# Performance work log

Measured on AMD Instinct MI355X. Metric: run time of the kernel, lower is better.

Reference implementation:

```python
import jax, jax.numpy as jnp
import numpy as np

V, E, H, B, S = 50257, 1024, 1024, 32, 1024

def setup_inputs() -> dict:
    key = jax.random.key(0)
    ks = jax.random.split(key, 16)
    s = 0.02
    return {
        "word_inputs": jax.random.randint(ks[0], (B, 1), 0, V),
        "hidden": jax.random.normal(ks[1], (1, B, H), jnp.float32),
        "output_encoder": jax.random.normal(ks[2], (B, S, H), jnp.float32),
        "emb": jax.random.normal(ks[3], (V, E), jnp.float32) * 0.2,
        "W_a1": jax.random.normal(ks[4], (H, 2 * H), jnp.float32) * s,
        "b_a1": jnp.zeros((H,), jnp.float32),
        "W_a2": jax.random.normal(ks[5], (1, H), jnp.float32) * s,
        "b_a2": jnp.zeros((1,), jnp.float32),
        "W_c": jax.random.normal(ks[6], (H, 2 * H), jnp.float32) * s,
        "b_c": jnp.zeros((H,), jnp.float32),
        "W_ih": jax.random.normal(ks[7], (3 * H, E), jnp.float32) * s,
        "W_hh": jax.random.normal(ks[8], (3 * H, H), jnp.float32) * s,
        "b_ih": jnp.zeros((3 * H,), jnp.float32),
        "b_hh": jnp.zeros((3 * H,), jnp.float32),
        "W_fc": jax.random.normal(ks[9], (V, H), jnp.float32) * 0.2,
        "b_fc": jnp.zeros((V,), jnp.float32),
    }

def reference(word_inputs, hidden, output_encoder, emb, W_a1, b_a1, W_a2, b_a2,
              W_c, b_c, W_ih, W_hh, b_ih, b_hh, W_fc, b_fc):
    b, s, h = output_encoder.shape
    h_prev = hidden[0]                                      # [B,H]
    # Bahdanau additive attention, vectorized over all S timesteps
    eh = jnp.concatenate(
        [output_encoder, jnp.broadcast_to(h_prev[:, None, :], (b, s, h))],
        axis=-1)                                            # [B,S,2H]
    scores = jnp.tanh(jnp.einsum('bsk,hk->bsh', eh, W_a1) + b_a1)
    scores = (jnp.einsum('bsh,oh->bso', scores, W_a2) + b_a2)[..., 0]  # [B,S]
    attn = jax.nn.softmax(scores, axis=1)                   # [B,S]
    context = jnp.einsum('bs,bsh->bh', attn, output_encoder)  # [B,H]
    embedded = emb[word_inputs.reshape(-1)]                 # [B,E]
    ec = jnp.concatenate([embedded, context], axis=-1)      # [B,E+H]
    x = jax.nn.relu(ec @ W_c.T + b_c)                       # [B,H]
    # single-step GRU (PyTorch gate order: r, z, n)
    gi = x @ W_ih.T + b_ih                                  # [B,3H]
    gh = h_prev @ W_hh.T + b_hh                             # [B,3H]
    i_r, i_z, i_n = jnp.split(gi, 3, axis=-1)
    h_r, h_z, h_n = jnp.split(gh, 3, axis=-1)
    r = jax.nn.sigmoid(i_r + h_r)
    z = jax.nn.sigmoid(i_z + h_z)
    n = jnp.tanh(i_n + r * h_n)
    h_new = (1.0 - z) * n + z * h_prev                      # [B,H]
    out = jax.nn.relu(h_new) @ W_fc.T + b_fc                # [B,V]
    return out, h_new[None, :, :]
```

## Files before the change

kernel.cpp:

```cpp
#include <hip/hip_runtime.h>

#define B_  32
#define S_  1024
#define H_  1024
#define V_  50257

typedef __attribute__((ext_vector_type(8))) short bf16x8;
typedef __attribute__((ext_vector_type(4))) float f32x4;
typedef __attribute__((ext_vector_type(8))) unsigned short u16x8;

__device__ __forceinline__ unsigned short f2b(float f) {
  union { float f; unsigned u; } v; v.f = f;
  unsigned r = 0x7FFFu + ((v.u >> 16) & 1u);
  return (unsigned short)((v.u + r) >> 16);
}
__device__ __forceinline__ float b2f(unsigned short h) {
  union { unsigned u; float f; } v; v.u = ((unsigned)h) << 16;
  return v.f;
}

__device__ __forceinline__ void async16(void* lds, const void* g) {
  typedef __attribute__((address_space(3))) void as3_void;
  typedef __attribute__((address_space(1))) void as1_void;
  as3_void* l = (as3_void*)(unsigned)(unsigned long long)lds;
  const as1_void* s = (const as1_void*)(unsigned long long)g;
  __builtin_amdgcn_global_load_lds(s, l, 16, 0, 0);
}

__global__ void prologue_kernel(const float* __restrict__ enc, unsigned short* __restrict__ enc_bf,
                                const float* __restrict__ wa1, const float* __restrict__ hidden,
                                const float* __restrict__ b_a1,
                                unsigned short* __restrict__ wa1_bf, float* __restrict__ part2) {
  __shared__ float wrow[H_];
  int tid = threadIdx.x;
  if (blockIdx.x < 16384) {
    size_t i = ((size_t)blockIdx.x * 256 + tid) * 8;
    float4 v0 = *(const float4*)(enc + i);
    float4 v1 = *(const float4*)(enc + i + 4);
    u16x8 o;
    o[0]=f2b(v0.x); o[1]=f2b(v0.y); o[2]=f2b(v0.z); o[3]=f2b(v0.w);
    o[4]=f2b(v1.x); o[5]=f2b(v1.y); o[6]=f2b(v1.z); o[7]=f2b(v1.w);
    *(u16x8*)(enc_bf + i) = o;
    return;
  }
  int h = blockIdx.x - 16384;
  {
    int c = tid * 4;
    float4 v = *(const float4*)(wa1 + (size_t)h * 2048 + c);
    ushort4 o;
    o.x = f2b(v.x); o.y = f2b(v.y); o.z = f2b(v.z); o.w = f2b(v.w);
    *(ushort4*)(wa1_bf + (size_t)h * 1024 + c) = o;
  }
  {
    int c = tid * 4;
    float4 v = *(const float4*)(wa1 + (size_t)h * 2048 + 1024 + c);
    wrow[c] = v.x; wrow[c+1] = v.y; wrow[c+2] = v.z; wrow[c+3] = v.w;
  }
  __syncthreads();
  int wave = tid >> 6, lane = tid & 63;
  float bias = b_a1[h];
  for (int bb = 0; bb < 8; ++bb) {
    int b = wave * 8 + bb;
    float acc = 0.f;
    for (int k = lane; k < H_; k += 64) acc += wrow[k] * hidden[b * H_ + k];
    #pragma unroll
    for (int off = 32; off; off >>= 1) acc += __shfl_xor(acc, off);
    if (lane == 0) part2[b * H_ + h] = acc + bias;
  }
}

__global__ __launch_bounds__(256) void scores_m97(
    const unsigned short* __restrict__ A,
    const unsigned short* __restrict__ Bm,
    const float* __restrict__ part2,
    const float* __restrict__ wa2,
    float* __restrict__ partials)
{
  __shared__ __align__(16) unsigned short As[2048];
  __shared__ __align__(16) unsigned short Bs[4096];
  const int tid = threadIdx.x;
  const int wave = tid >> 6, lane = tid & 63;
  const int wr = wave >> 1, wc = wave & 1;
  const int l15 = lane & 15, l16 = lane >> 4;

  const int id = blockIdx.x;
  const int xcd = id & 7;
  const int s = id >> 3;
  const int bm = (s >> 3) * 8 + xcd;
  const int bn = s & 7;

  const unsigned short* Abase = A  + (size_t)(bm * 64) * 1024;
  const unsigned short* Bbase = Bm + (size_t)(bn * 128) * 1024;

  const int Lc = tid * 16;
  const int r0 = Lc >> 6;
  const int ce0 = ((Lc & 63) ^ (((r0 >> 1) & 3) << 4)) >> 1;

  f32x4 acc[2][4];
  #pragma unroll
  for (int mi = 0; mi < 2; ++mi)
    #pragma unroll
    for (int ni = 0; ni < 4; ++ni) acc[mi][ni] = (f32x4){0.f, 0.f, 0.f, 0.f};
  bf16x8 af[2], bfr[4];

  for (int kt = 0; kt < 1024; kt += 32) {
    async16((char*)As + Lc,        Abase + (size_t)r0 * 1024 + kt + ce0);
    async16((char*)Bs + Lc,        Bbase + (size_t)r0 * 1024 + kt + ce0);
    async16((char*)Bs + Lc + 4096, Bbase + (size_t)(r0 + 64) * 1024 + kt + ce0);
    asm volatile("s_waitcnt vmcnt(0)" ::: "memory");
    __syncthreads();
    #pragma unroll
    for (int mi = 0; mi < 2; ++mi) {
      int ar = wr * 32 + mi * 16 + l15;
      int L = ar * 64 + l16 * 16;
      af[mi] = *(const bf16x8*)((const char*)As + (L ^ (((ar >> 1) & 3) << 4)));
    }
    #pragma unroll
    for (int ni = 0; ni < 4; ++ni) {
      int br = wc * 64 + ni * 16 + l15;
      int L = br * 64 + l16 * 16;
      bfr[ni] = *(const bf16x8*)((const char*)Bs + (L ^ (((br >> 1) & 3) << 4)));
    }
    #pragma unroll
    for (int mi = 0; mi < 2; ++mi)
      #pragma unroll
      for (int ni = 0; ni < 4; ++ni)
        acc[mi][ni] = __builtin_amdgcn_mfma_f32_16x16x32_bf16(af[mi], bfr[ni], acc[mi][ni], 0, 0, 0);
    __syncthreads();
  }

  const int b = bm >> 4;
  float w2[4], p2[4];
  #pragma unroll
  for (int ni = 0; ni < 4; ++ni) {
    int col = bn * 128 + wc * 64 + ni * 16 + l15;
    w2[ni] = wa2[col];
    p2[ni] = part2[b * H_ + col];
  }
  #pragma unroll
  for (int mi = 0; mi < 2; ++mi) {
    #pragma unroll
    for (int r = 0; r < 4; ++r) {
      float s2 = 0.f;
      #pragma unroll
      for (int ni = 0; ni < 4; ++ni)
        s2 += w2[ni] * tanhf(acc[mi][ni][r] + p2[ni]);
      s2 += __shfl_xor(s2, 1); s2 += __shfl_xor(s2, 2);
      s2 += __shfl_xor(s2, 4); s2 += __shfl_xor(s2, 8);
      if (l15 == 0) {
        int row = bm * 64 + wr * 32 + mi * 16 + l16 * 4 + r;
        partials[(size_t)row * 16 + bn * 2 + wc] = s2;
      }
    }
  }
}

__global__ __launch_bounds__(256) void smctx_kernel(
    const float* __restrict__ partials, const unsigned short* __restrict__ encbf,
    float* __restrict__ ctxp) {
  int sc = blockIdx.x, b = blockIdx.y, tid = threadIdx.x;
  int lane = tid & 63, wid = tid >> 6;
  __shared__ float att[1024];
  __shared__ float red[4];
  float scv[4];
  float mx = -1e30f;
  #pragma unroll
  for (int j = 0; j < 4; ++j) {
    int r = tid * 4 + j;
    const float4* p = (const float4*)(partials + ((size_t)b * 1024 + r) * 16);
    float s = 0.f;
    #pragma unroll
    for (int i = 0; i < 4; ++i) { float4 v = p[i]; s += v.x + v.y + v.z + v.w; }
    scv[j] = s; mx = fmaxf(mx, s);
  }
  #pragma unroll
  for (int off = 32; off; off >>= 1) mx = fmaxf(mx, __shfl_xor(mx, off));
  if (lane == 0) red[wid] = mx;
  __syncthreads();
  float M = fmaxf(fmaxf(red[0], red[1]), fmaxf(red[2], red[3]));
  float ssum = 0.f;
  #pragma unroll
  for (int j = 0; j < 4; ++j) { float e = expf(scv[j] - M); att[tid*4+j] = e; ssum += e; }
  #pragma unroll
  for (int off = 32; off; off >>= 1) ssum += __shfl_xor(ssum, off);
  __syncthreads();
  if (lane == 0) red[wid] = ssum;
  __syncthreads();
  float inv = 1.f / (red[0] + red[1] + red[2] + red[3]);
  int h4 = tid * 4;
  float a0 = 0, a1 = 0, a2 = 0, a3 = 0;
  const unsigned short* base = encbf + (size_t)b * S_ * H_ + h4;
  #pragma unroll 4
  for (int i = 0; i < 64; ++i) {
    float w = att[sc * 64 + i] * inv;
    ushort4 ev = *(const ushort4*)(base + (size_t)(sc * 64 + i) * H_);
    a0 += w * b2f(ev.x); a1 += w * b2f(ev.y); a2 += w * b2f(ev.z); a3 += w * b2f(ev.w);
  }
  float4 o = {a0, a1, a2, a3};
  *(float4*)(ctxp + (size_t)(sc * B_ + b) * H_ + h4) = o;
}

__global__ __launch_bounds__(256) void wc_gemm(
    const int* __restrict__ word, const float* __restrict__ emb,
    const float* __restrict__ ctxp, const float* __restrict__ Wc,
    float* __restrict__ xp) {
  int nb = blockIdx.x, kc = blockIdx.y, tid = threadIdx.x;
  __shared__ unsigned short A_lds[32][136];
  {
    int b = tid >> 3, cg = tid & 7;
    int c0 = cg * 16;
    if (kc < 8) {
      int w = word[b];
      const float* er = emb + (size_t)w * H_ + kc * 128 + c0;
      #pragma unroll
      for (int c = 0; c < 16; c += 4) {
        float4 v = *(const float4*)(er + c);
        ushort4 o; o.x = f2b(v.x); o.y = f2b(v.y); o.z = f2b(v.z); o.w = f2b(v.w);
        *(ushort4*)&A_lds[b][c0 + c] = o;
      }
    } else {
      int h0 = (kc - 8) * 128 + c0;
      #pragma unroll
      for (int c = 0; c < 16; c += 4) {
        float s0 = 0, s1 = 0, s2 = 0, s3 = 0;
        #pragma unroll
        for (int sc = 0; sc < 16; ++sc) {
          float4 v = *(const float4*)(ctxp + ((size_t)(sc * B_ + b)) * H_ + h0 + c);
          s0 += v.x; s1 += v.y; s2 += v.z; s3 += v.w;
        }
        ushort4 o; o.x = f2b(s0); o.y = f2b(s1); o.z = f2b(s2); o.w = f2b(s3);
        *(ushort4*)&A_lds[b][c0 + c] = o;
      }
    }
  }
  __syncthreads();
  int wave = tid >> 6, lane = tid & 63, l15 = lane & 15, l16 = lane >> 4;
  int col = nb * 64 + wave * 16 + l15;
  const float* bp = Wc + (size_t)col * 2048 + kc * 128 + l16 * 8;
  f32x4 acc0 = {0.f,0.f,0.f,0.f}, acc1 = {0.f,0.f,0.f,0.f};
  #pragma unroll
  for (int k = 0; k < 128; k += 32) {
    bf16x8 a0 = *(const bf16x8*)&A_lds[l15][k + l16 * 8];
    bf16x8 a1 = *(const bf16x8*)&A_lds[16 + l15][k + l16 * 8];
    float4 bv0 = *(const float4*)(bp + k);
    float4 bv1 = *(const float4*)(bp + k + 4);
    bf16x8 bb;
    bb[0] = (short)f2b(bv0.x); bb[1] = (short)f2b(bv0.y);
    bb[2] = (short)f2b(bv0.z); bb[3] = (short)f2b(bv0.w);
    bb[4] = (short)f2b(bv1.x); bb[5] = (short)f2b(bv1.y);
    bb[6] = (short)f2b(bv1.z); bb[7] = (short)f2b(bv1.w);
    acc0 = __builtin_amdgcn_mfma_f32_16x16x32_bf16(a0, bb, acc0, 0, 0, 0);
    acc1 = __builtin_amdgcn_mfma_f32_16x16x32_bf16(a1, bb, acc1, 0, 0, 0);
  }
  #pragma unroll
  for (int r = 0; r < 4; ++r) {
    int m = l16 * 4 + r;
    xp[(size_t)(kc * 32 + m) * H_ + col] = acc0[r];
    xp[(size_t)(kc * 32 + 16 + m) * H_ + col] = acc1[r];
  }
}

__global__ __launch_bounds__(256) void ihhh_gemm(
    const float* __restrict__ xp, const float* __restrict__ b_c,
    const float* __restrict__ hidden,
    const float* __restrict__ W_ih, const float* __restrict__ W_hh,
    float* __restrict__ gip, float* __restrict__ ghp) {
  int nb = blockIdx.x, kc = blockIdx.y, z = blockIdx.z, tid = threadIdx.x;
  __shared__ unsigned short A_lds[32][136];
  {
    int b = tid >> 3, cg = tid & 7;
    int c0 = cg * 16;
    int h0 = kc * 128 + c0;
    if (z == 0) {
      #pragma unroll
      for (int c = 0; c < 16; c += 4) {
        float4 bias = *(const float4*)(b_c + h0 + c);
        float s0 = bias.x, s1 = bias.y, s2 = bias.z, s3 = bias.w;
        #pragma unroll
        for (int sc = 0; sc < 16; ++sc) {
          float4 v = *(const float4*)(xp + ((size_t)(sc * B_ + b)) * H_ + h0 + c);
          s0 += v.x; s1 += v.y; s2 += v.z; s3 += v.w;
        }
        ushort4 o;
        o.x = f2b(fmaxf(s0, 0.f)); o.y = f2b(fmaxf(s1, 0.f));
        o.z = f2b(fmaxf(s2, 0.f)); o.w = f2b(fmaxf(s3, 0.f));
        *(ushort4*)&A_lds[b][c0 + c] = o;
      }
    } else {
      #pragma unroll
      for (int c = 0; c < 16; c += 4) {
        float4 v = *(const float4*)(hidden + (size_t)b * H_ + h0 + c);
        ushort4 o; o.x = f2b(v.x); o.y = f2b(v.y); o.z = f2b(v.z); o.w = f2b(v.w);
        *(ushort4*)&A_lds[b][c0 + c] = o;
      }
    }
  }
  __syncthreads();
  const float* Bw = z ? W_hh : W_ih;
  float* C = z ? ghp : gip;
  int wave = tid >> 6, lane = tid & 63, l15 = lane & 15, l16 = lane >> 4;
  int col = nb * 64 + wave * 16 + l15;
  const float* bp = Bw + (size_t)col * 1024 + kc * 128 + l16 * 8;
  f32x4 acc0 = {0.f,0.f,0.f,0.f}, acc1 = {0.f,0.f,0.f,0.f};
  #pragma unroll
  for (int k = 0; k < 128; k += 32) {
    bf16x8 a0 = *(const bf16x8*)&A_lds[l15][k + l16 * 8];
    bf16x8 a1 = *(const bf16x8*)&A_lds[16 + l15][k + l16 * 8];
    float4 bv0 = *(const float4*)(bp + k);
    float4 bv1 = *(const float4*)(bp + k + 4);
    bf16x8 bb;
    bb[0] = (short)f2b(bv0.x); bb[1] = (short)f2b(bv0.y);
    bb[2] = (short)f2b(bv0.z); bb[3] = (short)f2b(bv0.w);
    bb[4] = (short)f2b(bv1.x); bb[5] = (short)f2b(bv1.y);
    bb[6] = (short)f2b(bv1.z); bb[7] = (short)f2b(bv1.w);
    acc0 = __builtin_amdgcn_mfma_f32_16x16x32_bf16(a0, bb, acc0, 0, 0, 0);
    acc1 = __builtin_amdgcn_mfma_f32_16x16x32_bf16(a1, bb, acc1, 0, 0, 0);
  }
  #pragma unroll
  for (int r = 0; r < 4; ++r) {
    int m = l16 * 4 + r;
    C[(size_t)(kc * 32 + m) * 3072 + col] = acc0[r];
    C[(size_t)(kc * 32 + 16 + m) * 3072 + col] = acc1[r];
  }
}

__global__ void gates_kernel(const float* __restrict__ gip, const float* __restrict__ ghp,
                             const float* __restrict__ b_ih, const float* __restrict__ b_hh,
                             const float* __restrict__ hidden, float* __restrict__ hnew_out,
                             unsigned short* __restrict__ hr_bf) {
  int i = blockIdx.x * 256 + threadIdx.x;
  int b = i >> 10, h = i & 1023;
  float g[6];
  #pragma unroll
  for (int t = 0; t < 3; ++t) {
    int j = h + t * H_;
    float vi = b_ih[j], vh = b_hh[j];
    #pragma unroll
    for (int kc = 0; kc < 8; ++kc) {
      vi += gip[(size_t)(kc * B_ + b) * 3072 + j];
      vh += ghp[(size_t)(kc * B_ + b) * 3072 + j];
    }
    g[t] = vi; g[3 + t] = vh;
  }
  float r = 1.f / (1.f + expf(-(g[0] + g[3])));
  float z = 1.f / (1.f + expf(-(g[1] + g[4])));
  float n = tanhf(g[2] + r * g[5]);
  float hv = (1.f - z) * n + z * hidden[i];
  hnew_out[i] = hv;
  hr_bf[i] = f2b(hv > 0.f ? hv : 0.f);
}

__global__ __launch_bounds__(256) void fc_gemm(
    const unsigned short* __restrict__ A, const float* __restrict__ Bw,
    float* __restrict__ C, const float* __restrict__ bias) {
  const int N = V_, K = 1024;
  int n0 = blockIdx.x * 64;
  int wave = threadIdx.x >> 6, lane = threadIdx.x & 63;
  int l15 = lane & 15, l16 = lane >> 4;
  int col = n0 + wave * 16 + l15;
  int vclamp = col < N ? col : N - 1;
  const unsigned short* a0p = A + l15 * K + l16 * 8;
  const unsigned short* a1p = A + (16 + l15) * K + l16 * 8;
  const float* bp = Bw + (size_t)vclamp * K + l16 * 8;
  f32x4 acc0 = {0.f,0.f,0.f,0.f}, acc1 = {0.f,0.f,0.f,0.f};
  #pragma unroll 4
  for (int k = 0; k < K; k += 32) {
    bf16x8 a0 = *(const bf16x8*)(a0p + k);
    bf16x8 a1 = *(const bf16x8*)(a1p + k);
    float4 bv0 = *(const float4*)(bp + k);
    float4 bv1 = *(const float4*)(bp + k + 4);
    bf16x8 bb;
    bb[0] = (short)f2b(bv0.x); bb[1] = (short)f2b(bv0.y);
    bb[2] = (short)f2b(bv0.z); bb[3] = (short)f2b(bv0.w);
    bb[4] = (short)f2b(bv1.x); bb[5] = (short)f2b(bv1.y);
    bb[6] = (short)f2b(bv1.z); bb[7] = (short)f2b(bv1.w);
    acc0 = __builtin_amdgcn_mfma_f32_16x16x32_bf16(a0, bb, acc0, 0, 0, 0);
    acc1 = __builtin_amdgcn_mfma_f32_16x16x32_bf16(a1, bb, acc1, 0, 0, 0);
  }
  if (col < N) {
    float bv = bias[col];
    #pragma unroll
    for (int r = 0; r < 4; ++r) {
      int m = l16 * 4 + r;
      C[(size_t)m * N + col] = acc0[r] + bv;
      C[(size_t)(16 + m) * N + col] = acc1[r] + bv;
    }
  }
}

extern "C" void kernel_launch(void* const* d_in, const int* in_sizes, int n_in,
                              void* d_out, int out_size, void* d_ws, size_t ws_size,
                              hipStream_t stream) {
  const int*   word   = (const int*)  d_in[0];
  const float* hidden = (const float*)d_in[1];
  const float* enc    = (const float*)d_in[2];
  const float* emb    = (const float*)d_in[3];
  const float* W_a1   = (const float*)d_in[4];
  const float* b_a1   = (const float*)d_in[5];
  const float* W_a2   = (const float*)d_in[6];
  const float* b_c    = (const float*)d_in[9];
  const float* W_c    = (const float*)d_in[8];
  const float* W_ih   = (const float*)d_in[10];
  const float* W_hh   = (const float*)d_in[11];
  const float* b_ih   = (const float*)d_in[12];
  const float* b_hh   = (const float*)d_in[13];
  const float* W_fc   = (const float*)d_in[14];
  const float* b_fc   = (const float*)d_in[15];
  float* out = (float*)d_out;

  if (ws_size < 73596928ull) return;

  char* ws = (char*)d_ws;
  unsigned short* enc_bf   = (unsigned short*)(ws + 0);
  float*          gip      = (float*)         (ws + 0);
  float*          ghp      = (float*)         (ws + 3145728);
  unsigned short* wa1_bf   = (unsigned short*)(ws + 67108864);
  float*          xp       = (float*)         (ws + 67108864);
  float*          part2    = (float*)         (ws + 69206016);
  float*          partials = (float*)         (ws + 69337088);
  float*          ctxp     = (float*)         (ws + 71434240);
  unsigned short* hr_bf    = (unsigned short*)(ws + 73531392);

  prologue_kernel<<<dim3(17408), dim3(256), 0, stream>>>(enc, enc_bf, W_a1, hidden, b_a1,
                                                         wa1_bf, part2);
  scores_m97<<<dim3(4096), dim3(256), 0, stream>>>(enc_bf, wa1_bf, part2, W_a2, partials);
  smctx_kernel<<<dim3(16, 32), dim3(256), 0, stream>>>(partials, enc_bf, ctxp);
  wc_gemm<<<dim3(16, 16), dim3(256), 0, stream>>>(word, emb, ctxp, W_c, xp);
  ihhh_gemm<<<dim3(48, 8, 2), dim3(256), 0, stream>>>(xp, b_c, hidden, W_ih, W_hh, gip, ghp);
  gates_kernel<<<dim3(128), dim3(256), 0, stream>>>(gip, ghp, b_ih, b_hh, hidden,
                                                    out + (size_t)B_ * V_, hr_bf);
  fc_gemm<<<dim3(786), dim3(256), 0, stream>>>(hr_bf, W_fc, out, b_fc);
}
```

Measured before the change: 299.3 us.

## Double-buffer scores GEMM LDS loads and hoist x reduction into separate kernel

```diff
diff --git a/kernel.cpp b/kernel.cpp
--- a/kernel.cpp
+++ b/kernel.cpp
@@ -69,15 +69,15 @@
   }
 }
 
-__global__ __launch_bounds__(256) void scores_m97(
+__global__ __launch_bounds__(256) void scores_db(
     const unsigned short* __restrict__ A,
     const unsigned short* __restrict__ Bm,
     const float* __restrict__ part2,
     const float* __restrict__ wa2,
     float* __restrict__ partials)
 {
-  __shared__ __align__(16) unsigned short As[2048];
-  __shared__ __align__(16) unsigned short Bs[4096];
+  __shared__ __align__(16) unsigned short As[2][2048];
+  __shared__ __align__(16) unsigned short Bs[2][4096];
   const int tid = threadIdx.x;
   const int wave = tid >> 6, lane = tid & 63;
   const int wr = wave >> 1, wc = wave & 1;
@@ -96,6 +96,12 @@
   const int r0 = Lc >> 6;
   const int ce0 = ((Lc & 63) ^ (((r0 >> 1) & 3) << 4)) >> 1;
 
+  auto stage = [&](int kt, int db) {
+    async16((char*)As[db] + Lc,        Abase + (size_t)r0 * 1024 + kt + ce0);
+    async16((char*)Bs[db] + Lc,        Bbase + (size_t)r0 * 1024 + kt + ce0);
+    async16((char*)Bs[db] + Lc + 4096, Bbase + (size_t)(r0 + 64) * 1024 + kt + ce0);
+  };
+
   f32x4 acc[2][4];
   #pragma unroll
   for (int mi = 0; mi < 2; ++mi)
@@ -103,29 +109,32 @@
     for (int ni = 0; ni < 4; ++ni) acc[mi][ni] = (f32x4){0.f, 0.f, 0.f, 0.f};
   bf16x8 af[2], bfr[4];
 
-  for (int kt = 0; kt < 1024; kt += 32) {
-    async16((char*)As + Lc,        Abase + (size_t)r0 * 1024 + kt + ce0);
-    async16((char*)Bs + Lc,        Bbase + (size_t)r0 * 1024 + kt + ce0);
-    async16((char*)Bs + Lc + 4096, Bbase + (size_t)(r0 + 64) * 1024 + kt + ce0);
-    asm volatile("s_waitcnt vmcnt(0)" ::: "memory");
-    __syncthreads();
+  stage(0, 0);
+  asm volatile("s_waitcnt vmcnt(0)" ::: "memory");
+  __syncthreads();
+
+  #pragma unroll 1
+  for (int t = 0; t < 32; ++t) {
+    const int buf = t & 1;
+    if (t < 31) stage((t + 1) * 32, buf ^ 1);
     #pragma unroll
     for (int mi = 0; mi < 2; ++mi) {
       int ar = wr * 32 + mi * 16 + l15;
       int L = ar * 64 + l16 * 16;
-      af[mi] = *(const bf16x8*)((const char*)As + (L ^ (((ar >> 1) & 3) << 4)));
+      af[mi] = *(const bf16x8*)((const char*)As[buf] + (L ^ (((ar >> 1) & 3) << 4)));
     }
     #pragma unroll
     for (int ni = 0; ni < 4; ++ni) {
       int br = wc * 64 + ni * 16 + l15;
       int L = br * 64 + l16 * 16;
-      bfr[ni] = *(const bf16x8*)((const char*)Bs + (L ^ (((br >> 1) & 3) << 4)));
+      bfr[ni] = *(const bf16x8*)((const char*)Bs[buf] + (L ^ (((br >> 1) & 3) << 4)));
     }
     #pragma unroll
     for (int mi = 0; mi < 2; ++mi)
       #pragma unroll
       for (int ni = 0; ni < 4; ++ni)
         acc[mi][ni] = __builtin_amdgcn_mfma_f32_16x16x32_bf16(af[mi], bfr[ni], acc[mi][ni], 0, 0, 0);
+    asm volatile("s_waitcnt vmcnt(0)" ::: "memory");
     __syncthreads();
   }
 
@@ -260,9 +269,18 @@
   }
 }
 
+__global__ void xfinish_kernel(const float* __restrict__ xp, const float* __restrict__ b_c,
+                               unsigned short* __restrict__ x_bf) {
+  int i = blockIdx.x * 256 + threadIdx.x;
+  int b = i >> 10, h = i & 1023;
+  float v = b_c[h];
+  #pragma unroll
+  for (int kc = 0; kc < 16; ++kc) v += xp[(size_t)(kc * B_ + b) * H_ + h];
+  x_bf[i] = f2b(v > 0.f ? v : 0.f);
+}
+
 __global__ __launch_bounds__(256) void ihhh_gemm(
-    const float* __restrict__ xp, const float* __restrict__ b_c,
-    const float* __restrict__ hidden,
+    const unsigned short* __restrict__ x_bf, const float* __restrict__ hidden,
     const float* __restrict__ W_ih, const float* __restrict__ W_hh,
     float* __restrict__ gip, float* __restrict__ ghp) {
   int nb = blockIdx.x, kc = blockIdx.y, z = blockIdx.z, tid = threadIdx.x;
@@ -273,18 +291,9 @@
     int h0 = kc * 128 + c0;
     if (z == 0) {
       #pragma unroll
-      for (int c = 0; c < 16; c += 4) {
-        float4 bias = *(const float4*)(b_c + h0 + c);
-        float s0 = bias.x, s1 = bias.y, s2 = bias.z, s3 = bias.w;
-        #pragma unroll
-        for (int sc = 0; sc < 16; ++sc) {
-          float4 v = *(const float4*)(xp + ((size_t)(sc * B_ + b)) * H_ + h0 + c);
-          s0 += v.x; s1 += v.y; s2 += v.z; s3 += v.w;
-        }
-        ushort4 o;
-        o.x = f2b(fmaxf(s0, 0.f)); o.y = f2b(fmaxf(s1, 0.f));
-        o.z = f2b(fmaxf(s2, 0.f)); o.w = f2b(fmaxf(s3, 0.f));
-        *(ushort4*)&A_lds[b][c0 + c] = o;
+      for (int c = 0; c < 16; c += 8) {
+        u16x8 v = *(const u16x8*)(x_bf + (size_t)b * H_ + h0 + c);
+        *(u16x8*)&A_lds[b][c0 + c] = v;
       }
     } else {
       #pragma unroll
@@ -408,7 +417,7 @@
   const float* b_fc   = (const float*)d_in[15];
   float* out = (float*)d_out;
 
-  if (ws_size < 73596928ull) return;
+  if (ws_size < 73662464ull) return;
 
   char* ws = (char*)d_ws;
   unsigned short* enc_bf   = (unsigned short*)(ws + 0);
@@ -420,13 +429,15 @@
   float*          partials = (float*)         (ws + 69337088);
   float*          ctxp     = (float*)         (ws + 71434240);
   unsigned short* hr_bf    = (unsigned short*)(ws + 73531392);
+  unsigned short* x_bf     = (unsigned short*)(ws + 73596928);
 
   prologue_kernel<<<dim3(17408), dim3(256), 0, stream>>>(enc, enc_bf, W_a1, hidden, b_a1,
                                                          wa1_bf, part2);
-  scores_m97<<<dim3(4096), dim3(256), 0, stream>>>(enc_bf, wa1_bf, part2, W_a2, partials);
+  scores_db<<<dim3(4096), dim3(256), 0, stream>>>(enc_bf, wa1_bf, part2, W_a2, partials);
   smctx_kernel<<<dim3(16, 32), dim3(256), 0, stream>>>(partials, enc_bf, ctxp);
   wc_gemm<<<dim3(16, 16), dim3(256), 0, stream>>>(word, emb, ctxp, W_c, xp);
-  ihhh_gemm<<<dim3(48, 8, 2), dim3(256), 0, stream>>>(xp, b_c, hidden, W_ih, W_hh, gip, ghp);
+  xfinish_kernel<<<dim3(128), dim3(256), 0, stream>>>(xp, b_c, x_bf);
+  ihhh_gemm<<<dim3(48, 8, 2), dim3(256), 0, stream>>>(x_bf, hidden, W_ih, W_hh, gip, ghp);
   gates_kernel<<<dim3(128), dim3(256), 0, stream>>>(gip, ghp, b_ih, b_hh, hidden,
                                                     out + (size_t)B_ * V_, hr_bf);
   fc_gemm<<<dim3(786), dim3(256), 0, stream>>>(hr_bf, W_fc, out, b_fc);
```

Result: faster. 292.5 us (-2.3%).
